# Performance work log

Hardware: AMD Instinct MI355X
Metric: run time of the kernel (lower is better)

The kernel has to match this reference:

```python
import jax, jax.numpy as jnp
import numpy as np

N = 100000   # nodes
E = 800000   # edges
F = 64       # num_features == hidden_dim
D = 64       # hidden_dim
L = 3        # num_gc_layers
NG = 512     # num graphs in batch
BN_EPS = 1e-5


def setup_inputs() -> dict:
    key = jax.random.key(0)
    ks = jax.random.split(key, 16)
    s = 0.05
    return {
        "x": jax.random.normal(ks[0], (N, F), jnp.float32),
        "edge_index": jax.random.randint(ks[1], (2, E), 0, N),
        "batch": jnp.sort(jax.random.randint(ks[2], (N,), 0, NG)),
        "W1": jax.random.normal(ks[3], (L, F, D), jnp.float32) * s,
        "b1": jnp.zeros((L, D), jnp.float32),
        "W2": jax.random.normal(ks[4], (L, D, D), jnp.float32) * s,
        "b2": jnp.zeros((L, D), jnp.float32),
        "gin_eps": jnp.zeros((L,), jnp.float32),
        "gin_bias": jnp.zeros((L, D), jnp.float32),
        "bn_gamma": jnp.ones((L, D), jnp.float32),
        "bn_beta": jnp.zeros((L, D), jnp.float32),
        "Wp1": jax.random.normal(ks[5], (L * D, L * D), jnp.float32) * s,
        "bp1": jnp.zeros((L * D,), jnp.float32),
        "Wp2": jax.random.normal(ks[6], (L * D, L * D), jnp.float32) * s,
        "bp2": jnp.zeros((L * D,), jnp.float32),
    }


def reference(x, edge_index, batch, W1, b1, W2, b2, gin_eps, gin_bias,
              bn_gamma, bn_beta, Wp1, bp1, Wp2, bp2):
    row, col = edge_index[0], edge_index[1]
    h = x
    xs = []
    for i in range(L):
        # sparse adj @ h : sum over incoming edges (adj[row, col] = 1)
        agg = jax.ops.segment_sum(h[col], row, num_segments=N)
        z = (1.0 + gin_eps[i]) * h + agg
        # GIN internal MLP: Linear -> ReLU -> Linear -> ReLU
        z = jax.nn.relu(z @ W1[i] + b1[i])
        z = jax.nn.relu(z @ W2[i] + b2[i])
        # conv bias + relu (outer F.relu in Encoder is idempotent)
        z = jax.nn.relu(z + gin_bias[i])
        # BatchNorm1d, training mode: batch stats over nodes, biased variance
        mean = jnp.mean(z, axis=0)
        var = jnp.mean(jnp.square(z - mean), axis=0)
        h = (z - mean) * jax.lax.rsqrt(var + BN_EPS) * bn_gamma[i] + bn_beta[i]
        xs.append(h)
    # per-layer global add pool over graphs, then concat -> [NG, L*D]
    pooled = jnp.concatenate(
        [jax.ops.segment_sum(xi, batch, num_segments=NG) for xi in xs], axis=1)
    # projection head: Linear -> ReLU -> Linear
    y = jax.nn.relu(pooled @ Wp1 + bp1) @ Wp2 + bp2
    return y
```

## Files before the change

### kernel.cpp

```cpp
#include <hip/hip_runtime.h>

#define N_NODES 100000
#define N_EDGES 800000
#define DF 64
#define NGRAPH 512
#define LDIM 192
#define BN_EPS 1e-5
#define NTILES 6250
#define GIN_GRID 782
#define NWT (GIN_GRID * 8)
#define COLS_CAP 2600000
#define NBUCK 782
#define BCAP 2048
#define NBLK 128
#define CHUNK 6250

typedef __attribute__((ext_vector_type(8))) short bf16x8;
typedef __attribute__((ext_vector_type(4))) float f32x4;

__device__ inline short f2bf(float x) {
    union { float f; unsigned u; } v; v.f = x;
    unsigned r = v.u + 0x7fff + ((v.u >> 16) & 1);
    return (short)(r >> 16);
}

__device__ inline float bf2f(unsigned short u) {
    union { unsigned u; float f; } v;
    v.u = ((unsigned)u) << 16;
    return v.f;
}

__device__ inline int pdeg_of(int d) {
    int p = (d + 15) & ~15;
    return p < 16 ? 16 : p;
}

__global__ __launch_bounds__(256) void blk_hist_kernel(
    const int* __restrict__ ei, int* __restrict__ hist)
{
    __shared__ int hh[NBUCK];
    int blk = blockIdx.x, tid = threadIdx.x;
    for (int i = tid; i < NBUCK; i += 256) hh[i] = 0;
    __syncthreads();
    int start = blk * CHUNK, end = min(start + CHUNK, N_EDGES);
    for (int e = start + tid; e < end; e += 256)
        atomicAdd(&hh[ei[e] >> 7], 1);
    __syncthreads();
    for (int i = tid; i < NBUCK; i += 256) hist[blk * NBUCK + i] = hh[i];
}

__global__ __launch_bounds__(NBLK) void blk_scan_kernel(
    const int* __restrict__ hist, int* __restrict__ pos, int* __restrict__ cnt)
{
    __shared__ int buf[NBLK];
    int k = blockIdx.x, b = threadIdx.x;
    int v = hist[b * NBUCK + k];
    buf[b] = v;
    __syncthreads();
    for (int o = 1; o < NBLK; o <<= 1) {
        int t = (b >= o) ? buf[b - o] : 0;
        __syncthreads();
        buf[b] += t;
        __syncthreads();
    }
    pos[b * NBUCK + k] = buf[b] - v;
    if (b == NBLK - 1) cnt[k] = buf[b];
}

__global__ __launch_bounds__(256) void place_kernel(
    const int* __restrict__ ei, const int* __restrict__ pos,
    unsigned* __restrict__ bucketData)
{
    __shared__ int cursor[NBUCK];
    int blk = blockIdx.x, tid = threadIdx.x;
    for (int i = tid; i < NBUCK; i += 256) cursor[i] = pos[blk * NBUCK + i];
    __syncthreads();
    int start = blk * CHUNK, end = min(start + CHUNK, N_EDGES);
    for (int e = start + tid; e < end; e += 256) {
        int r = ei[e];
        int c = ei[N_EDGES + e];
        int k = r >> 7;
        int p = atomicAdd(&cursor[k], 1);
        bucketData[(size_t)k * BCAP + p] = ((unsigned)(r & 127) << 17) | (unsigned)c;
    }
}

__global__ __launch_bounds__(256) void bucket_count_kernel(
    const unsigned* __restrict__ bucketData, const int* __restrict__ cnt,
    int* __restrict__ deg, int* __restrict__ bpad)
{
    __shared__ int rc[128];
    __shared__ int red[4];
    int b = blockIdx.x, tid = threadIdx.x;
    int rowbase = b << 7;
    int nrows = min(128, N_NODES - rowbase);
    int cntb = cnt[b];
    if (tid < 128) rc[tid] = 0;
    __syncthreads();
    for (int e = tid; e < cntb; e += 256)
        atomicAdd(&rc[bucketData[(size_t)b * BCAP + e] >> 17], 1);
    __syncthreads();
    int v = 0;
    if (tid < nrows) {
        int d = rc[tid];
        deg[rowbase + tid] = d;
        v = pdeg_of(d);
    }
    #pragma unroll
    for (int o = 32; o > 0; o >>= 1) v += __shfl_down(v, o, 64);
    if ((tid & 63) == 0) red[tid >> 6] = v;
    __syncthreads();
    if (tid == 0) bpad[b] = red[0] + red[1] + red[2] + red[3];
}

__global__ __launch_bounds__(1024) void bucket_scan_kernel(
    const int* __restrict__ bpad, int* __restrict__ bbase)
{
    __shared__ int buf[1024];
    int tid = threadIdx.x;
    int own = (tid < NBUCK) ? bpad[tid] : 0;
    buf[tid] = own;
    __syncthreads();
    for (int o = 1; o < 1024; o <<= 1) {
        int t = (tid >= o) ? buf[tid - o] : 0;
        __syncthreads();
        buf[tid] += t;
        __syncthreads();
    }
    if (tid < NBUCK) bbase[tid] = buf[tid] - own;
}

__global__ __launch_bounds__(256) void bucket_emit_kernel(
    const unsigned* __restrict__ bucketData, const int* __restrict__ cnt,
    const int* __restrict__ bbase,
    int* __restrict__ off, int* __restrict__ colS)
{
    __shared__ int rc[128], rstart[128], rcur[128], sbuf[128];
    __shared__ int region[4096];
    int b = blockIdx.x, tid = threadIdx.x;
    int rowbase = b << 7;
    int nrows = min(128, N_NODES - rowbase);
    int cntb = cnt[b];
    int base = bbase[b];
    if (tid < 128) rc[tid] = 0;
    __syncthreads();
    for (int e = tid; e < cntb; e += 256)
        atomicAdd(&rc[bucketData[(size_t)b * BCAP + e] >> 17], 1);
    __syncthreads();
    int pd = (tid < nrows) ? pdeg_of(rc[tid]) : 0;
    if (tid < 128) sbuf[tid] = pd;
    __syncthreads();
    for (int o = 1; o < 128; o <<= 1) {
        int t = 0;
        if (tid < 128 && tid >= o) t = sbuf[tid - o];
        __syncthreads();
        if (tid < 128) sbuf[tid] += t;
        __syncthreads();
    }
    if (tid < 128) { rstart[tid] = sbuf[tid] - pd; rcur[tid] = sbuf[tid] - pd; }
    __syncthreads();
    int total = sbuf[127];
    for (int e = tid; e < cntb; e += 256) {
        unsigned p = bucketData[(size_t)b * BCAP + e];
        int lr = p >> 17;
        int c = p & 0x1FFFF;
        int pos = atomicAdd(&rcur[lr], 1);
        region[pos] = c * DF;
    }
    __syncthreads();
    for (int i = tid; i < nrows; i += 256) {
        int st = rstart[i] + rc[i];
        int en = rstart[i] + pdeg_of(rc[i]);
        int sent = (rowbase + i) * DF;
        for (int j = st; j < en; ++j) region[j] = sent;
    }
    __syncthreads();
    for (int k = tid; k < total; k += 256) colS[base + k] = region[k];
    if (tid < nrows) off[rowbase + tid] = base + rstart[tid];
    if (b == NBUCK - 1 && tid == 0) off[N_NODES] = base + total;
}

__global__ __launch_bounds__(256) void gstart_kernel(
    const int* __restrict__ batch, int* __restrict__ gstart,
    float* __restrict__ idsc, float* __restrict__ idsh)
{
    int g = blockIdx.x * 256 + threadIdx.x;
    if (g < 64) { idsc[g] = 1.0f; idsh[g] = 0.0f; }
    if (g > NGRAPH) return;
    if (g == NGRAPH) { gstart[g] = N_NODES; return; }
    int lo = 0, hi = N_NODES;
    while (lo < hi) {
        int mid = (lo + hi) >> 1;
        if (batch[mid] < g) lo = mid + 1; else hi = mid;
    }
    gstart[g] = lo;
}

__global__ __launch_bounds__(256) void pack_w_kernel(
    const float* __restrict__ W1, const float* __restrict__ W2,
    short* __restrict__ Wpk)
{
    int u = blockIdx.x;
    int layer = u >> 1, gm = u & 1;
    const float* W = (gm ? W2 : W1) + layer * 4096;
    short* dst = Wpk + u * 4096;
    for (int idx = threadIdx.x; idx < 4096; idx += 256) {
        int i = idx & 7;
        int l = (idx >> 3) & 63;
        int rest = idx >> 9;
        int kt = rest & 1, nt = rest >> 1;
        int k = kt * 32 + (l >> 4) * 8 + i;
        int n = nt * 16 + (l & 15);
        dst[idx] = f2bf(W[k * 64 + n]);
    }
}

template <bool BF16IN>
__global__ __launch_bounds__(512) void gin_layer_kernel(
    const void* __restrict__ zp_,
    const float* __restrict__ sc_in,
    const float* __restrict__ sh_in,
    const int* __restrict__ off,
    const int* __restrict__ deg,
    const int* __restrict__ colS,
    unsigned short* __restrict__ zout,
    const short* __restrict__ Wpk,
    const float* __restrict__ b1,
    const float* __restrict__ b2,
    const float* __restrict__ gin_eps,
    const float* __restrict__ gin_bias,
    float* __restrict__ part_s,
    float* __restrict__ part_q)
{
    __shared__ __align__(16) short Wp1s[4096];
    __shared__ __align__(16) short Wp2s[4096];
    __shared__ __align__(16) short zs[8][16 * 72];

    const float* zpf = (const float*)zp_;
    const unsigned short* zpb = (const unsigned short*)zp_;

    int tid = threadIdx.x;
    {
        const short4* s1 = (const short4*)Wpk;
        const short4* s2 = (const short4*)(Wpk + 4096);
        short4* d1 = (short4*)Wp1s;
        short4* d2 = (short4*)Wp2s;
        for (int i = tid; i < 1024; i += 512) { d1[i] = s1[i]; d2[i] = s2[i]; }
    }

    int w = tid >> 6, l = tid & 63;
    int lr = l & 15;
    int lk = l >> 4;
    float epsf = 1.0f + gin_eps[0];
    float scf = sc_in[l], shf = sh_in[l];
    float b1f[4], b2f[4], gbf[4];
    #pragma unroll
    for (int nt = 0; nt < 4; ++nt) {
        b1f[nt] = b1[nt * 16 + lr];
        b2f[nt] = b2[nt * 16 + lr];
        gbf[nt] = gin_bias[nt * 16 + lr];
    }
    float ssum[4] = {0, 0, 0, 0}, sq[4] = {0, 0, 0, 0};
    short* zw = zs[w];
    __syncthreads();

    int t = blockIdx.x * 8 + w;
    bool active = t < NTILES;
    int n0 = t * 16;

    if (active) {
        #pragma unroll 1
        for (int mp = 0; mp < 8; ++mp) {
            int nodeA = n0 + (mp << 1);
            int nodeB = nodeA + 1;
            int sA = __builtin_amdgcn_readfirstlane(off[nodeA]);
            int eA = __builtin_amdgcn_readfirstlane(off[nodeA + 1]);
            int dA = __builtin_amdgcn_readfirstlane(deg[nodeA]);
            int sB = __builtin_amdgcn_readfirstlane(off[nodeB]);
            int eB = __builtin_amdgcn_readfirstlane(off[nodeB + 1]);
            int dB = __builtin_amdgcn_readfirstlane(deg[nodeB]);
            float hnA, hnB;
            if (BF16IN) { hnA = bf2f(zpb[nodeA * DF + l]); hnB = bf2f(zpb[nodeB * DF + l]); }
            else        { hnA = zpf[nodeA * DF + l];       hnB = zpf[nodeB * DF + l]; }
            float vA[16], vB[16];
            #pragma unroll
            for (int j = 0; j < 16; ++j) {
                int co = __builtin_amdgcn_readfirstlane(colS[sA + j]);
                vA[j] = BF16IN ? bf2f(zpb[co + l]) : zpf[co + l];
            }
            #pragma unroll
            for (int j = 0; j < 16; ++j) {
                int co = __builtin_amdgcn_readfirstlane(colS[sB + j]);
                vB[j] = BF16IN ? bf2f(zpb[co + l]) : zpf[co + l];
            }
            float aA0 = (vA[0] + vA[1]) + (vA[2] + vA[3]);
            float aA1 = (vA[4] + vA[5]) + (vA[6] + vA[7]);
            float aA2 = (vA[8] + vA[9]) + (vA[10] + vA[11]);
            float aA3 = (vA[12] + vA[13]) + (vA[14] + vA[15]);
            float accA = (aA0 + aA1) + (aA2 + aA3);
            float aB0 = (vB[0] + vB[1]) + (vB[2] + vB[3]);
            float aB1 = (vB[4] + vB[5]) + (vB[6] + vB[7]);
            float aB2 = (vB[8] + vB[9]) + (vB[10] + vB[11]);
            float aB3 = (vB[12] + vB[13]) + (vB[14] + vB[15]);
            float accB = (aB0 + aB1) + (aB2 + aB3);
            for (int i = sA + 16; i < eA; i += 16) {
                #pragma unroll
                for (int j = 0; j < 16; ++j) {
                    int co = __builtin_amdgcn_readfirstlane(colS[i + j]);
                    accA += BF16IN ? bf2f(zpb[co + l]) : zpf[co + l];
                }
            }
            for (int i = sB + 16; i < eB; i += 16) {
                #pragma unroll
                for (int j = 0; j < 16; ++j) {
                    int co = __builtin_amdgcn_readfirstlane(colS[i + j]);
                    accB += BF16IN ? bf2f(zpb[co + l]) : zpf[co + l];
                }
            }
            float npA = (float)(eA - sA - dA);
            float npB = (float)(eB - sB - dB);
            float zfA = scf * ((epsf - npA) * hnA + accA) + (epsf + (float)dA) * shf;
            float zfB = scf * ((epsf - npB) * hnB + accB) + (epsf + (float)dB) * shf;
            zw[(mp * 2) * 72 + l] = f2bf(zfA);
            zw[(mp * 2 + 1) * 72 + l] = f2bf(zfB);
        }

        {
            bf16x8 a0 = *(const bf16x8*)&zw[lr * 72 + lk * 8];
            bf16x8 a1 = *(const bf16x8*)&zw[lr * 72 + 32 + lk * 8];
            #pragma unroll
            for (int nt = 0; nt < 4; ++nt) {
                f32x4 acc = {0.f, 0.f, 0.f, 0.f};
                bf16x8 bb0 = *(const bf16x8*)&Wp1s[((nt * 2 + 0) * 64 + l) * 8];
                bf16x8 bb1 = *(const bf16x8*)&Wp1s[((nt * 2 + 1) * 64 + l) * 8];
                acc = __builtin_amdgcn_mfma_f32_16x16x32_bf16(a0, bb0, acc, 0, 0, 0);
                acc = __builtin_amdgcn_mfma_f32_16x16x32_bf16(a1, bb1, acc, 0, 0, 0);
                #pragma unroll
                for (int r = 0; r < 4; ++r) {
                    float v = fmaxf(acc[r] + b1f[nt], 0.0f);
                    zw[(lk * 4 + r) * 72 + nt * 16 + lr] = f2bf(v);
                }
            }
        }

        {
            bf16x8 a0 = *(const bf16x8*)&zw[lr * 72 + lk * 8];
            bf16x8 a1 = *(const bf16x8*)&zw[lr * 72 + 32 + lk * 8];
            #pragma unroll
            for (int nt = 0; nt < 4; ++nt) {
                f32x4 acc = {0.f, 0.f, 0.f, 0.f};
                bf16x8 bb0 = *(const bf16x8*)&Wp2s[((nt * 2 + 0) * 64 + l) * 8];
                bf16x8 bb1 = *(const bf16x8*)&Wp2s[((nt * 2 + 1) * 64 + l) * 8];
                acc = __builtin_amdgcn_mfma_f32_16x16x32_bf16(a0, bb0, acc, 0, 0, 0);
                acc = __builtin_amdgcn_mfma_f32_16x16x32_bf16(a1, bb1, acc, 0, 0, 0);
                #pragma unroll
                for (int r = 0; r < 4; ++r) {
                    float v = fmaxf(fmaxf(acc[r] + b2f[nt], 0.0f) + gbf[nt], 0.0f);
                    unsigned short vb = (unsigned short)f2bf(v);
                    zout[(n0 + lk * 4 + r) * DF + nt * 16 + lr] = vb;
                    float vr = bf2f(vb);
                    ssum[nt] += vr;
                    sq[nt] += vr * vr;
                }
            }
        }
    }

    #pragma unroll
    for (int nt = 0; nt < 4; ++nt) {
        float sv = ssum[nt], qv = sq[nt];
        sv += __shfl_xor(sv, 16, 64); sv += __shfl_xor(sv, 32, 64);
        qv += __shfl_xor(qv, 16, 64); qv += __shfl_xor(qv, 32, 64);
        if (l < 16) {
            part_s[(nt * 16 + l) * NWT + t] = sv;
            part_q[(nt * 16 + l) * NWT + t] = qv;
        }
    }
}

__global__ __launch_bounds__(256) void stat_reduce_kernel(
    const float* __restrict__ part_s, const float* __restrict__ part_q,
    const float* __restrict__ gamma, const float* __restrict__ beta,
    float* __restrict__ scale, float* __restrict__ shift)
{
    __shared__ double rs[4], rq[4];
    int f = blockIdx.x, tid = threadIdx.x;
    double s = 0.0, q = 0.0;
    for (int j = tid; j < NWT; j += 256) {
        s += (double)part_s[f * NWT + j];
        q += (double)part_q[f * NWT + j];
    }
    for (int o = 32; o > 0; o >>= 1) {
        s += __shfl_down(s, o, 64);
        q += __shfl_down(q, o, 64);
    }
    if ((tid & 63) == 0) { rs[tid >> 6] = s; rq[tid >> 6] = q; }
    __syncthreads();
    if (tid == 0) {
        double st = rs[0] + rs[1] + rs[2] + rs[3];
        double qt = rq[0] + rq[1] + rq[2] + rq[3];
        double mean = st / N_NODES;
        double var = qt / N_NODES - mean * mean;
        double inv = (double)gamma[f] / sqrt(var + BN_EPS);
        scale[f] = (float)inv;
        shift[f] = (float)((double)beta[f] - mean * inv);
    }
}

__global__ __launch_bounds__(256) void pool_kernel(
    const unsigned short* __restrict__ z,
    const float* __restrict__ scale,
    const float* __restrict__ shift,
    const int* __restrict__ gstart,
    float* __restrict__ pooled,
    int layerOff)
{
    __shared__ float red[4][64];
    int g = blockIdx.x;
    int tid = threadIdx.x;
    int w = tid >> 6, f = tid & 63;

    int s = gstart[g], e = gstart[g + 1];
    float acc = 0.0f;
    for (int node = s + w; node < e; node += 4)
        acc += bf2f(z[node * DF + f]);
    red[w][f] = acc;
    __syncthreads();
    if (w == 0)
        pooled[g * LDIM + layerOff + f] =
            scale[f] * (red[0][f] + red[1][f] + red[2][f] + red[3][f])
            + (float)(e - s) * shift[f];
}

__global__ __launch_bounds__(192) void proj_fused_kernel(
    const float* __restrict__ in,
    const float* __restrict__ Wp1, const float* __restrict__ bp1,
    const float* __restrict__ Wp2, const float* __restrict__ bp2,
    float* __restrict__ out)
{
    __shared__ float rowS[LDIM];
    __shared__ float hid[LDIM];
    int r = blockIdx.x;
    int c = threadIdx.x;
    rowS[c] = in[r * LDIM + c];
    __syncthreads();
    float acc = bp1[c];
    #pragma unroll 4
    for (int k = 0; k < LDIM; ++k) acc += rowS[k] * Wp1[k * LDIM + c];
    hid[c] = fmaxf(acc, 0.0f);
    __syncthreads();
    float acc2 = bp2[c];
    #pragma unroll 4
    for (int k = 0; k < LDIM; ++k) acc2 += hid[k] * Wp2[k * LDIM + c];
    out[r * LDIM + c] = acc2;
}

extern "C" void kernel_launch(void* const* d_in, const int* in_sizes, int n_in,
                              void* d_out, int out_size, void* d_ws, size_t ws_size,
                              hipStream_t stream)
{
    const float* x        = (const float*)d_in[0];
    const int*   ei       = (const int*)d_in[1];
    const int*   batch    = (const int*)d_in[2];
    const float* W1       = (const float*)d_in[3];
    const float* b1       = (const float*)d_in[4];
    const float* W2       = (const float*)d_in[5];
    const float* b2       = (const float*)d_in[6];
    const float* gin_eps  = (const float*)d_in[7];
    const float* gin_bias = (const float*)d_in[8];
    const float* gamma    = (const float*)d_in[9];
    const float* beta     = (const float*)d_in[10];
    const float* Wp1      = (const float*)d_in[11];
    const float* bp1      = (const float*)d_in[12];
    const float* Wp2      = (const float*)d_in[13];
    const float* bp2      = (const float*)d_in[14];
    float* out = (float*)d_out;

    unsigned short* zbufA = (unsigned short*)d_ws;
    unsigned short* zbufB = zbufA + (size_t)N_NODES * DF;
    float* pooled = (float*)(zbufB + (size_t)N_NODES * DF);
    float* scale = pooled + (size_t)NGRAPH * LDIM;
    float* shift = scale + 64;
    float* idsc = shift + 64;
    float* idsh = idsc + 64;
    float* part_s = idsh + 64;
    float* part_q = part_s + (size_t)64 * NWT;
    int* gstart = (int*)(part_q + (size_t)64 * NWT);
    int* deg  = gstart + NGRAPH + 1;
    int* off  = deg + N_NODES;
    int* colS = off + N_NODES + 1;
    int* hist = colS + COLS_CAP;
    int* pos  = hist + NBLK * NBUCK;
    int* cnt  = pos + NBLK * NBUCK;
    int* bpad = cnt + NBUCK;
    int* bbase = bpad + NBUCK;
    unsigned* bucketData = (unsigned*)(bbase + NBUCK);
    short* Wpk = (short*)(bucketData + (size_t)NBUCK * BCAP);

    blk_hist_kernel<<<NBLK, 256, 0, stream>>>(ei, hist);
    blk_scan_kernel<<<NBUCK, NBLK, 0, stream>>>(hist, pos, cnt);
    place_kernel<<<NBLK, 256, 0, stream>>>(ei, pos, bucketData);
    bucket_count_kernel<<<NBUCK, 256, 0, stream>>>(bucketData, cnt, deg, bpad);
    bucket_scan_kernel<<<1, 1024, 0, stream>>>(bpad, bbase);
    bucket_emit_kernel<<<NBUCK, 256, 0, stream>>>(bucketData, cnt, bbase,
                                                  off, colS);
    gstart_kernel<<<3, 256, 0, stream>>>(batch, gstart, idsc, idsh);
    pack_w_kernel<<<6, 256, 0, stream>>>(W1, W2, Wpk);

    unsigned short* zbuf[2] = {zbufA, zbufB};
    const void* zprev = (const void*)x;
    const float* sc_in = idsc;
    const float* sh_in = idsh;
    for (int l = 0; l < 3; ++l) {
        unsigned short* zcur = zbuf[l & 1];
        if (l == 0)
            gin_layer_kernel<false><<<GIN_GRID, 512, 0, stream>>>(
                zprev, sc_in, sh_in, off, deg, colS, zcur,
                Wpk + (size_t)l * 8192,
                b1 + l * 64, b2 + l * 64, gin_eps + l, gin_bias + l * 64,
                part_s, part_q);
        else
            gin_layer_kernel<true><<<GIN_GRID, 512, 0, stream>>>(
                zprev, sc_in, sh_in, off, deg, colS, zcur,
                Wpk + (size_t)l * 8192,
                b1 + l * 64, b2 + l * 64, gin_eps + l, gin_bias + l * 64,
                part_s, part_q);

        stat_reduce_kernel<<<64, 256, 0, stream>>>(
            part_s, part_q, gamma + l * 64, beta + l * 64, scale, shift);

        pool_kernel<<<NGRAPH, 256, 0, stream>>>(
            zcur, scale, shift, gstart, pooled, l * 64);

        zprev = (const void*)zcur;
        sc_in = scale;
        sh_in = shift;
    }

    proj_fused_kernel<<<NGRAPH, LDIM, 0, stream>>>(pooled, Wp1, bp1, Wp2, bp2, out);
}
```

Measured before the change: 278.5 us.

## Interleave adjacency in 8-row packs and gather 16-byte bf16 rows per lane

```diff
diff --git a/kernel.cpp b/kernel.cpp
--- a/kernel.cpp
+++ b/kernel.cpp
@@ -9,11 +9,13 @@
 #define NTILES 6250
 #define GIN_GRID 782
 #define NWT (GIN_GRID * 8)
+#define NPACKS 12500
 #define COLS_CAP 2600000
 #define NBUCK 782
 #define BCAP 2048
 #define NBLK 128
 #define CHUNK 6250
+#define REGION_CAP 6144
 
 typedef __attribute__((ext_vector_type(8))) short bf16x8;
 typedef __attribute__((ext_vector_type(4))) float f32x4;
@@ -23,16 +25,34 @@
     unsigned r = v.u + 0x7fff + ((v.u >> 16) & 1);
     return (short)(r >> 16);
 }
-
 __device__ inline float bf2f(unsigned short u) {
-    union { unsigned u; float f; } v;
-    v.u = ((unsigned)u) << 16;
-    return v.f;
-}
-
-__device__ inline int pdeg_of(int d) {
-    int p = (d + 15) & ~15;
-    return p < 16 ? 16 : p;
+    union { unsigned u; float f; } v; v.u = ((unsigned)u) << 16; return v.f;
+}
+__device__ inline float bflo(unsigned u) {
+    union { unsigned x; float f; } v; v.x = u << 16; return v.f;
+}
+__device__ inline float bfhi(unsigned u) {
+    union { unsigned x; float f; } v; v.x = u & 0xffff0000u; return v.f;
+}
+
+__global__ __launch_bounds__(256) void x2bf_kernel(
+    const float* __restrict__ x, unsigned short* __restrict__ xb)
+{
+    int i = blockIdx.x * 256 + threadIdx.x;
+    const int total = N_NODES * DF / 8;
+    if (i >= total) return;
+    const float4* src = (const float4*)(x + (size_t)i * 8);
+    float4 a = src[0], b = src[1];
+    unsigned short u0 = (unsigned short)f2bf(a.x), u1 = (unsigned short)f2bf(a.y);
+    unsigned short u2 = (unsigned short)f2bf(a.z), u3 = (unsigned short)f2bf(a.w);
+    unsigned short u4 = (unsigned short)f2bf(b.x), u5 = (unsigned short)f2bf(b.y);
+    unsigned short u6 = (unsigned short)f2bf(b.z), u7 = (unsigned short)f2bf(b.w);
+    uint4 o;
+    o.x = (unsigned)u0 | ((unsigned)u1 << 16);
+    o.y = (unsigned)u2 | ((unsigned)u3 << 16);
+    o.z = (unsigned)u4 | ((unsigned)u5 << 16);
+    o.w = (unsigned)u6 | ((unsigned)u7 << 16);
+    ((uint4*)xb)[i] = o;
 }
 
 __global__ __launch_bounds__(256) void blk_hist_kernel(
@@ -90,7 +110,7 @@
     int* __restrict__ deg, int* __restrict__ bpad)
 {
     __shared__ int rc[128];
-    __shared__ int red[4];
+    __shared__ int wps[16];
     int b = blockIdx.x, tid = threadIdx.x;
     int rowbase = b << 7;
     int nrows = min(128, N_NODES - rowbase);
@@ -100,17 +120,20 @@
     for (int e = tid; e < cntb; e += 256)
         atomicAdd(&rc[bucketData[(size_t)b * BCAP + e] >> 17], 1);
     __syncthreads();
-    int v = 0;
-    if (tid < nrows) {
-        int d = rc[tid];
-        deg[rowbase + tid] = d;
-        v = pdeg_of(d);
-    }
-    #pragma unroll
-    for (int o = 32; o > 0; o >>= 1) v += __shfl_down(v, o, 64);
-    if ((tid & 63) == 0) red[tid >> 6] = v;
-    __syncthreads();
-    if (tid == 0) bpad[b] = red[0] + red[1] + red[2] + red[3];
+    if (tid < nrows) deg[rowbase + tid] = rc[tid];
+    if (tid < 16) {
+        int m = 0;
+        #pragma unroll
+        for (int i = 0; i < 8; ++i) m = max(m, rc[tid * 8 + i]);
+        wps[tid] = (m + 1) & ~1;
+    }
+    __syncthreads();
+    if (tid == 0) {
+        int s = 0;
+        #pragma unroll
+        for (int pk = 0; pk < 16; ++pk) s += 8 * wps[pk];
+        bpad[b] = s;
+    }
 }
 
 __global__ __launch_bounds__(1024) void bucket_scan_kernel(
@@ -133,51 +156,59 @@
 __global__ __launch_bounds__(256) void bucket_emit_kernel(
     const unsigned* __restrict__ bucketData, const int* __restrict__ cnt,
     const int* __restrict__ bbase,
-    int* __restrict__ off, int* __restrict__ colS)
-{
-    __shared__ int rc[128], rstart[128], rcur[128], sbuf[128];
-    __shared__ int region[4096];
+    int* __restrict__ colT, int* __restrict__ offT, int* __restrict__ widT)
+{
+    __shared__ int rc[128], rcur[128];
+    __shared__ int wps[16], pstart[16];
+    __shared__ int region[REGION_CAP];
+    __shared__ int totalS;
     int b = blockIdx.x, tid = threadIdx.x;
     int rowbase = b << 7;
     int nrows = min(128, N_NODES - rowbase);
     int cntb = cnt[b];
     int base = bbase[b];
-    if (tid < 128) rc[tid] = 0;
+    if (tid < 128) { rc[tid] = 0; rcur[tid] = 0; }
     __syncthreads();
     for (int e = tid; e < cntb; e += 256)
         atomicAdd(&rc[bucketData[(size_t)b * BCAP + e] >> 17], 1);
     __syncthreads();
-    int pd = (tid < nrows) ? pdeg_of(rc[tid]) : 0;
-    if (tid < 128) sbuf[tid] = pd;
-    __syncthreads();
-    for (int o = 1; o < 128; o <<= 1) {
-        int t = 0;
-        if (tid < 128 && tid >= o) t = sbuf[tid - o];
-        __syncthreads();
-        if (tid < 128) sbuf[tid] += t;
-        __syncthreads();
-    }
-    if (tid < 128) { rstart[tid] = sbuf[tid] - pd; rcur[tid] = sbuf[tid] - pd; }
-    __syncthreads();
-    int total = sbuf[127];
+    if (tid < 16) {
+        int m = 0;
+        #pragma unroll
+        for (int i = 0; i < 8; ++i) m = max(m, rc[tid * 8 + i]);
+        wps[tid] = (m + 1) & ~1;
+    }
+    __syncthreads();
+    if (tid == 0) {
+        int run = 0;
+        #pragma unroll
+        for (int pk = 0; pk < 16; ++pk) { pstart[pk] = run; run += 8 * wps[pk]; }
+        totalS = run;
+    }
+    __syncthreads();
+    int total = totalS;
     for (int e = tid; e < cntb; e += 256) {
         unsigned p = bucketData[(size_t)b * BCAP + e];
         int lr = p >> 17;
         int c = p & 0x1FFFF;
-        int pos = atomicAdd(&rcur[lr], 1);
-        region[pos] = c * DF;
+        int slot = atomicAdd(&rcur[lr], 1);
+        int pk = lr >> 3, g = lr & 7;
+        region[pstart[pk] + slot * 8 + g] = c * DF;
     }
     __syncthreads();
     for (int i = tid; i < nrows; i += 256) {
-        int st = rstart[i] + rc[i];
-        int en = rstart[i] + pdeg_of(rc[i]);
+        int pk = i >> 3, g = i & 7;
+        int wp = wps[pk];
         int sent = (rowbase + i) * DF;
-        for (int j = st; j < en; ++j) region[j] = sent;
-    }
-    __syncthreads();
-    for (int k = tid; k < total; k += 256) colS[base + k] = region[k];
-    if (tid < nrows) off[rowbase + tid] = base + rstart[tid];
-    if (b == NBUCK - 1 && tid == 0) off[N_NODES] = base + total;
+        for (int slot = rc[i]; slot < wp; ++slot)
+            region[pstart[pk] + slot * 8 + g] = sent;
+    }
+    __syncthreads();
+    for (int k = tid; k < total; k += 256) colT[base + k] = region[k];
+    if (tid < 16 && tid * 8 < nrows) {
+        offT[b * 16 + tid] = base + pstart[tid];
+        widT[b * 16 + tid] = wps[tid];
+    }
 }
 
 __global__ __launch_bounds__(256) void gstart_kernel(
@@ -215,14 +246,14 @@
     }
 }
 
-template <bool BF16IN>
 __global__ __launch_bounds__(512) void gin_layer_kernel(
-    const void* __restrict__ zp_,
+    const unsigned short* __restrict__ zpb,
     const float* __restrict__ sc_in,
     const float* __restrict__ sh_in,
-    const int* __restrict__ off,
+    const int* __restrict__ offT,
+    const int* __restrict__ widT,
     const int* __restrict__ deg,
-    const int* __restrict__ colS,
+    const int* __restrict__ colT,
     unsigned short* __restrict__ zout,
     const short* __restrict__ Wpk,
     const float* __restrict__ b1,
@@ -234,10 +265,7 @@
 {
     __shared__ __align__(16) short Wp1s[4096];
     __shared__ __align__(16) short Wp2s[4096];
-    __shared__ __align__(16) short zs[8][16 * 72];
-
-    const float* zpf = (const float*)zp_;
-    const unsigned short* zpb = (const unsigned short*)zp_;
+    __shared__ __align__(16) short zs[8][16 * 80];
 
     int tid = threadIdx.x;
     {
@@ -251,8 +279,9 @@
     int w = tid >> 6, l = tid & 63;
     int lr = l & 15;
     int lk = l >> 4;
+    int g8 = l >> 3;
+    int j8 = l & 7;
     float epsf = 1.0f + gin_eps[0];
-    float scf = sc_in[l], shf = sh_in[l];
     float b1f[4], b2f[4], gbf[4];
     #pragma unroll
     for (int nt = 0; nt < 4; ++nt) {
@@ -260,74 +289,69 @@
         b2f[nt] = b2[nt * 16 + lr];
         gbf[nt] = gin_bias[nt * 16 + lr];
     }
+    float4 sca = *(const float4*)&sc_in[j8 * 8];
+    float4 scb = *(const float4*)&sc_in[j8 * 8 + 4];
+    float4 sha = *(const float4*)&sh_in[j8 * 8];
+    float4 shb = *(const float4*)&sh_in[j8 * 8 + 4];
     float ssum[4] = {0, 0, 0, 0}, sq[4] = {0, 0, 0, 0};
     short* zw = zs[w];
     __syncthreads();
 
     int t = blockIdx.x * 8 + w;
     bool active = t < NTILES;
-    int n0 = t * 16;
 
     if (active) {
-        #pragma unroll 1
-        for (int mp = 0; mp < 8; ++mp) {
-            int nodeA = n0 + (mp << 1);
-            int nodeB = nodeA + 1;
-            int sA = __builtin_amdgcn_readfirstlane(off[nodeA]);
-            int eA = __builtin_amdgcn_readfirstlane(off[nodeA + 1]);
-            int dA = __builtin_amdgcn_readfirstlane(deg[nodeA]);
-            int sB = __builtin_amdgcn_readfirstlane(off[nodeB]);
-            int eB = __builtin_amdgcn_readfirstlane(off[nodeB + 1]);
-            int dB = __builtin_amdgcn_readfirstlane(deg[nodeB]);
-            float hnA, hnB;
-            if (BF16IN) { hnA = bf2f(zpb[nodeA * DF + l]); hnB = bf2f(zpb[nodeB * DF + l]); }
-            else        { hnA = zpf[nodeA * DF + l];       hnB = zpf[nodeB * DF + l]; }
-            float vA[16], vB[16];
+        #pragma unroll
+        for (int half = 0; half < 2; ++half) {
+            int p = t * 2 + half;
+            int nP0 = p * 8;
+            int sP = __builtin_amdgcn_readfirstlane(offT[p]);
+            int wP = __builtin_amdgcn_readfirstlane(widT[p]);
+            float acc[8];
             #pragma unroll
-            for (int j = 0; j < 16; ++j) {
-                int co = __builtin_amdgcn_readfirstlane(colS[sA + j]);
-                vA[j] = BF16IN ? bf2f(zpb[co + l]) : zpf[co + l];
+            for (int i = 0; i < 8; ++i) acc[i] = 0.0f;
+            #pragma unroll 1
+            for (int it = 0; it < wP; it += 2) {
+                int co0 = colT[sP + it * 8 + g8];
+                int co1 = colT[sP + it * 8 + 8 + g8];
+                uint4 v0 = *(const uint4*)(zpb + co0 + j8 * 8);
+                uint4 v1 = *(const uint4*)(zpb + co1 + j8 * 8);
+                acc[0] += bflo(v0.x) + bflo(v1.x);
+                acc[1] += bfhi(v0.x) + bfhi(v1.x);
+                acc[2] += bflo(v0.y) + bflo(v1.y);
+                acc[3] += bfhi(v0.y) + bfhi(v1.y);
+                acc[4] += bflo(v0.z) + bflo(v1.z);
+                acc[5] += bfhi(v0.z) + bfhi(v1.z);
+                acc[6] += bflo(v0.w) + bflo(v1.w);
+                acc[7] += bfhi(v0.w) + bfhi(v1.w);
             }
+            int node = nP0 + g8;
+            int d = deg[node];
+            uint4 hv = *(const uint4*)(zpb + node * DF + j8 * 8);
+            float hn[8] = { bflo(hv.x), bfhi(hv.x), bflo(hv.y), bfhi(hv.y),
+                            bflo(hv.z), bfhi(hv.z), bflo(hv.w), bfhi(hv.w) };
+            float np = (float)(wP - d);
+            float em = epsf - np;
+            float dh = epsf + (float)d;
+            float scv[8] = { sca.x, sca.y, sca.z, sca.w, scb.x, scb.y, scb.z, scb.w };
+            float shv[8] = { sha.x, sha.y, sha.z, sha.w, shb.x, shb.y, shb.z, shb.w };
+            unsigned short us[8];
             #pragma unroll
-            for (int j = 0; j < 16; ++j) {
-                int co = __builtin_amdgcn_readfirstlane(colS[sB + j]);
-                vB[j] = BF16IN ? bf2f(zpb[co + l]) : zpf[co + l];
+            for (int i = 0; i < 8; ++i) {
+                float zf = scv[i] * (em * hn[i] + acc[i]) + dh * shv[i];
+                us[i] = (unsigned short)f2bf(zf);
             }
-            float aA0 = (vA[0] + vA[1]) + (vA[2] + vA[3]);
-            float aA1 = (vA[4] + vA[5]) + (vA[6] + vA[7]);
-            float aA2 = (vA[8] + vA[9]) + (vA[10] + vA[11]);
-            float aA3 = (vA[12] + vA[13]) + (vA[14] + vA[15]);
-            float accA = (aA0 + aA1) + (aA2 + aA3);
-            float aB0 = (vB[0] + vB[1]) + (vB[2] + vB[3]);
-            float aB1 = (vB[4] + vB[5]) + (vB[6] + vB[7]);
-            float aB2 = (vB[8] + vB[9]) + (vB[10] + vB[11]);
-            float aB3 = (vB[12] + vB[13]) + (vB[14] + vB[15]);
-            float accB = (aB0 + aB1) + (aB2 + aB3);
-            for (int i = sA + 16; i < eA; i += 16) {
-                #pragma unroll
-                for (int j = 0; j < 16; ++j) {
-                    int co = __builtin_amdgcn_readfirstlane(colS[i + j]);
-                    accA += BF16IN ? bf2f(zpb[co + l]) : zpf[co + l];
-                }
-            }
-            for (int i = sB + 16; i < eB; i += 16) {
-                #pragma unroll
-                for (int j = 0; j < 16; ++j) {
-                    int co = __builtin_amdgcn_readfirstlane(colS[i + j]);
-                    accB += BF16IN ? bf2f(zpb[co + l]) : zpf[co + l];
-                }
-            }
-            float npA = (float)(eA - sA - dA);
-            float npB = (float)(eB - sB - dB);
-            float zfA = scf * ((epsf - npA) * hnA + accA) + (epsf + (float)dA) * shf;
-            float zfB = scf * ((epsf - npB) * hnB + accB) + (epsf + (float)dB) * shf;
-            zw[(mp * 2) * 72 + l] = f2bf(zfA);
-            zw[(mp * 2 + 1) * 72 + l] = f2bf(zfB);
+            uint4 zpk;
+            zpk.x = (unsigned)us[0] | ((unsigned)us[1] << 16);
+            zpk.y = (unsigned)us[2] | ((unsigned)us[3] << 16);
+            zpk.z = (unsigned)us[4] | ((unsigned)us[5] << 16);
+            zpk.w = (unsigned)us[6] | ((unsigned)us[7] << 16);
+            *(uint4*)&zw[(half * 8 + g8) * 80 + j8 * 8] = zpk;
         }
 
         {
-            bf16x8 a0 = *(const bf16x8*)&zw[lr * 72 + lk * 8];
-            bf16x8 a1 = *(const bf16x8*)&zw[lr * 72 + 32 + lk * 8];
+            bf16x8 a0 = *(const bf16x8*)&zw[lr * 80 + lk * 8];
+            bf16x8 a1 = *(const bf16x8*)&zw[lr * 80 + 32 + lk * 8];
             #pragma unroll
             for (int nt = 0; nt < 4; ++nt) {
                 f32x4 acc = {0.f, 0.f, 0.f, 0.f};
@@ -338,14 +362,15 @@
                 #pragma unroll
                 for (int r = 0; r < 4; ++r) {
                     float v = fmaxf(acc[r] + b1f[nt], 0.0f);
-                    zw[(lk * 4 + r) * 72 + nt * 16 + lr] = f2bf(v);
+                    zw[(lk * 4 + r) * 80 + nt * 16 + lr] = f2bf(v);
                 }
             }
         }
 
         {
-            bf16x8 a0 = *(const bf16x8*)&zw[lr * 72 + lk * 8];
-            bf16x8 a1 = *(const bf16x8*)&zw[lr * 72 + 32 + lk * 8];
+            int n0 = t * 16;
+            bf16x8 a0 = *(const bf16x8*)&zw[lr * 80 + lk * 8];
+            bf16x8 a1 = *(const bf16x8*)&zw[lr * 80 + 32 + lk * 8];
             #pragma unroll
             for (int nt = 0; nt < 4; ++nt) {
                 f32x4 acc = {0.f, 0.f, 0.f, 0.f};
@@ -476,7 +501,8 @@
     const float* bp2      = (const float*)d_in[14];
     float* out = (float*)d_out;
 
-    unsigned short* zbufA = (unsigned short*)d_ws;
+    unsigned short* xb    = (unsigned short*)d_ws;
+    unsigned short* zbufA = xb + (size_t)N_NODES * DF;
     unsigned short* zbufB = zbufA + (size_t)N_NODES * DF;
     float* pooled = (float*)(zbufB + (size_t)N_NODES * DF);
     float* scale = pooled + (size_t)NGRAPH * LDIM;
@@ -487,9 +513,10 @@
     float* part_q = part_s + (size_t)64 * NWT;
     int* gstart = (int*)(part_q + (size_t)64 * NWT);
     int* deg  = gstart + NGRAPH + 1;
-    int* off  = deg + N_NODES;
-    int* colS = off + N_NODES + 1;
-    int* hist = colS + COLS_CAP;
+    int* offT = deg + N_NODES;
+    int* widT = offT + 16 * NBUCK;
+    int* colT = widT + 16 * NBUCK;
+    int* hist = colT + COLS_CAP;
     int* pos  = hist + NBLK * NBUCK;
     int* cnt  = pos + NBLK * NBUCK;
     int* bpad = cnt + NBUCK;
@@ -497,34 +524,28 @@
     unsigned* bucketData = (unsigned*)(bbase + NBUCK);
     short* Wpk = (short*)(bucketData + (size_t)NBUCK * BCAP);
 
+    x2bf_kernel<<<(N_NODES * DF / 8 + 255) / 256, 256, 0, stream>>>(x, xb);
     blk_hist_kernel<<<NBLK, 256, 0, stream>>>(ei, hist);
     blk_scan_kernel<<<NBUCK, NBLK, 0, stream>>>(hist, pos, cnt);
     place_kernel<<<NBLK, 256, 0, stream>>>(ei, pos, bucketData);
     bucket_count_kernel<<<NBUCK, 256, 0, stream>>>(bucketData, cnt, deg, bpad);
     bucket_scan_kernel<<<1, 1024, 0, stream>>>(bpad, bbase);
     bucket_emit_kernel<<<NBUCK, 256, 0, stream>>>(bucketData, cnt, bbase,
-                                                  off, colS);
+                                                  colT, offT, widT);
     gstart_kernel<<<3, 256, 0, stream>>>(batch, gstart, idsc, idsh);
     pack_w_kernel<<<6, 256, 0, stream>>>(W1, W2, Wpk);
 
     unsigned short* zbuf[2] = {zbufA, zbufB};
-    const void* zprev = (const void*)x;
+    const unsigned short* zprev = xb;
     const float* sc_in = idsc;
     const float* sh_in = idsh;
     for (int l = 0; l < 3; ++l) {
         unsigned short* zcur = zbuf[l & 1];
-        if (l == 0)
-            gin_layer_kernel<false><<<GIN_GRID, 512, 0, stream>>>(
-                zprev, sc_in, sh_in, off, deg, colS, zcur,
-                Wpk + (size_t)l * 8192,
-                b1 + l * 64, b2 + l * 64, gin_eps + l, gin_bias + l * 64,
-                part_s, part_q);
-        else
-            gin_layer_kernel<true><<<GIN_GRID, 512, 0, stream>>>(
-                zprev, sc_in, sh_in, off, deg, colS, zcur,
-                Wpk + (size_t)l * 8192,
-                b1 + l * 64, b2 + l * 64, gin_eps + l, gin_bias + l * 64,
-                part_s, part_q);
+        gin_layer_kernel<<<GIN_GRID, 512, 0, stream>>>(
+            zprev, sc_in, sh_in, offT, widT, deg, colT, zcur,
+            Wpk + (size_t)l * 8192,
+            b1 + l * 64, b2 + l * 64, gin_eps + l, gin_bias + l * 64,
+            part_s, part_q);
 
         stat_reduce_kernel<<<64, 256, 0, stream>>>(
             part_s, part_q, gamma + l * 64, beta + l * 64, scale, shift);
@@ -532,7 +553,7 @@
         pool_kernel<<<NGRAPH, 256, 0, stream>>>(
             zcur, scale, shift, gstart, pooled, l * 64);
 
-        zprev = (const void*)zcur;
+        zprev = zcur;
         sc_in = scale;
         sh_in = shift;
     }
```

New measurement: 272.3 us. -2.2%, faster.
